# Performance work log

Measured on AMD Instinct MI355X. Metric: run time of the kernel, lower is better.

The kernel has to match this reference:

```python
import jax, jax.numpy as jnp
import numpy as np

F_DIM = 2
L_LEVELS = 16
N_MIN, N_MAX = 16, 2048
_B = np.exp((np.log(N_MAX) - np.log(N_MIN)) / (L_LEVELS - 1))
NL = np.array([int(np.floor(N_MIN * _B ** l)) for l in range(L_LEVELS)], dtype=np.float32)
T_SIZE = 2 ** 19
AABB = 3.0
N_PTS = 262144
N_FREQ_DIR = 4  # direction PE frequencies -> 3 + 3*2*4 = 27 dims (matches color_MLP input 16+27)
PIS = np.array([1, 2654435761, 805459861], dtype=np.uint32)
# 8 cube-corner offsets; order matches the torch vertex enumeration
OFFS = np.array([[0,0,0],[1,0,0],[0,1,0],[1,1,0],[0,0,1],[1,0,1],[0,1,1],[1,1,1]], dtype=np.float32)


def _hash_encode(xn, tables):
    # xn: [N,3] normalized positions in ~[0,1); tables: [L,T,F]
    Ns = jnp.asarray(NL)                                   # [L]
    scaled = xn[None, :, :] * Ns[:, None, None]            # [L,N,3]
    fl = jnp.floor(scaled)
    loc = scaled - fl                                      # [L,N,3] trilinear weights
    offs_i = jnp.asarray(OFFS, jnp.int32)                  # [8,3]
    verts = fl.astype(jnp.int32)[:, :, None, :] + offs_i[None, None]   # [L,N,8,3]
    v = verts.astype(jnp.uint32)
    pis = jnp.asarray(PIS)
    h = ((v[..., 0] * pis[0]) ^ (v[..., 1] * pis[1]) ^ (v[..., 2] * pis[2])) % jnp.uint32(T_SIZE)
    idx = h.astype(jnp.int32)                              # [L,N,8]
    corner = jax.vmap(lambda t, i: t[i])(tables, idx)      # [L,N,8,F] hashed gather
    offs = jnp.asarray(OFFS)                               # [8,3]
    w = jnp.prod(offs[None, None] * loc[:, :, None, :] + (1.0 - offs[None, None]) * (1.0 - loc[:, :, None, :]), axis=-1)  # [L,N,8]
    feats = jnp.einsum('lnc,lncf->lnf', w, corner)         # [L,N,F]
    N = xn.shape[0]
    return feats.transpose(1, 0, 2).reshape(N, L_LEVELS * F_DIM)  # [N, L*F]


def _pos_enc_dir(d):
    outs = [d]
    for j in range(N_FREQ_DIR):
        outs.append(jnp.sin((2.0 ** j) * d))
        outs.append(jnp.cos((2.0 ** j) * d))
    return jnp.concatenate(outs, axis=1)                   # [N,27]


def setup_inputs() -> dict:
    key = jax.random.key(0)
    ks = jax.random.split(key, 12)
    x = jax.random.normal(ks[0], (N_PTS, 3), jnp.float32)
    d = jax.random.normal(ks[1], (N_PTS, 3), jnp.float32)
    tables = (jax.random.uniform(ks[2], (L_LEVELS, T_SIZE, F_DIM), jnp.float32) * 2.0 - 1.0) * 1e-4
    def lin(k, fi, fo):
        return jax.random.normal(k, (fi, fo), jnp.float32) * (1.0 / np.sqrt(fi))
    return {
        'x': x, 'd': d, 'tables': tables,
        'dW1': lin(ks[3], 32, 64), 'db1': jnp.zeros((64,), jnp.float32),
        'dW2': lin(ks[4], 64, 16), 'db2': jnp.zeros((16,), jnp.float32),
        'cW1': lin(ks[5], 43, 64), 'cb1': jnp.zeros((64,), jnp.float32),
        'cW2': lin(ks[6], 64, 64), 'cb2': jnp.zeros((64,), jnp.float32),
        'cW3': lin(ks[7], 64, 3), 'cb3': jnp.zeros((3,), jnp.float32),
    }


def reference(x, d, tables, dW1, db1, dW2, db2, cW1, cb1, cW2, cb2, cW3, cb3):
    xn = x / AABB
    mask = (jnp.abs(xn[:, 0]) < 0.5) & (jnp.abs(xn[:, 1]) < 0.5) & (jnp.abs(xn[:, 2]) < 0.5)
    xn = xn + 0.5
    feats = _hash_encode(xn, tables)                        # [N,32]
    h = jnp.maximum(feats @ dW1 + db1, 0.0) @ dW2 + db2     # [N,16]
    d_enc = _pos_enc_dir(d)                                 # [N,27]
    ch = jnp.concatenate([h, d_enc], axis=1)                # [N,43]
    ch = jnp.maximum(ch @ cW1 + cb1, 0.0)
    ch = jnp.maximum(ch @ cW2 + cb2, 0.0)
    rgb = jax.nn.sigmoid(ch @ cW3 + cb3)                    # [N,3]
    sigma = jnp.where(mask, h[:, 0], jnp.float32(-100000.0))
    rgb = jnp.where(mask[:, None], rgb, 0.0)
    return rgb, jnp.exp(sigma)
```

## Files before the change

### kernel.cpp

```cpp
#include <hip/hip_runtime.h>

#define NPTS 262144
#define HP1 2654435761u
#define HP2 805459861u
#define TMASK 0x7FFFFu

typedef __attribute__((ext_vector_type(8))) short short8;
typedef __attribute__((ext_vector_type(4))) float f32x4;
typedef unsigned short ushort_t;
typedef unsigned int uint_t;

#define MFMA(a, b, c) __builtin_amdgcn_mfma_f32_16x16x32_bf16((a), (b), (c), 0, 0, 0)

__device__ __forceinline__ ushort_t f2bf(float f) {
    uint_t u = __float_as_uint(f);
    return (ushort_t)((u + 0x7FFFu + ((u >> 16) & 1u)) >> 16);
}
__device__ __forceinline__ float sigmoidf_fast(float v) {
    return 1.0f / (1.0f + __expf(-v));
}

#define DOFF0 0
#define DOFF1 4913
#define DOFF2 17080
#define DOFF3 46871
#define DOFF4 126378
#define DTOT  331757

#define WS_DN_OFF (16u * 1024u * 1024u)
#define WS_WF_OFF (22u * 1024u * 1024u)

#define OFF_DW1 0
#define OFF_DW2 2048
#define OFF_CW1 3072
#define OFF_CW2 7168
#define OFF_CW3 11264
#define WF_TOTAL 12288

extern "C" __global__ void ngp_prep(
    const float* __restrict__ dW1, const float* __restrict__ dW2,
    const float* __restrict__ cW1, const float* __restrict__ cW2,
    const float* __restrict__ cW3, ushort_t* __restrict__ wf)
{
    const int e = blockIdx.x * 256 + (int)threadIdx.x;
    if (e >= WF_TOTAL) return;
    const float* W; int base, NT, KR, NR;
    if (e < OFF_DW2)      { W = dW1; base = OFF_DW1; NT = 4; KR = 32; NR = 64; }
    else if (e < OFF_CW1) { W = dW2; base = OFF_DW2; NT = 1; KR = 64; NR = 16; }
    else if (e < OFF_CW2) { W = cW1; base = OFF_CW1; NT = 4; KR = 43; NR = 64; }
    else if (e < OFF_CW3) { W = cW2; base = OFF_CW2; NT = 4; KR = 64; NR = 64; }
    else                  { W = cW3; base = OFF_CW3; NT = 1; KR = 64; NR = 3;  }
    const int r = e - base;
    const int frag = r >> 9;
    const int lane = (r >> 3) & 63;
    const int j = r & 7;
    const int kc = frag / NT, nt = frag % NT;
    const int k = kc * 32 + ((lane >> 4) << 3) + j;
    const int n = nt * 16 + (lane & 15);
    const float v = (k < KR && n < NR) ? W[k * NR + n] : 0.0f;
    wf[e] = f2bf(v);
}

extern "C" __global__ void ngp_dense(
    const float* __restrict__ tbl, f32x4* __restrict__ dense)
{
    const int e = blockIdx.x * 256 + (int)threadIdx.x;
    if (e >= DTOT) return;
    int l, base, dim;
    if (e < DOFF1)      { l = 0; base = DOFF0; dim = 17; }
    else if (e < DOFF2) { l = 1; base = DOFF1; dim = 23; }
    else if (e < DOFF3) { l = 2; base = DOFF2; dim = 31; }
    else if (e < DOFF4) { l = 3; base = DOFF3; dim = 43; }
    else                { l = 4; base = DOFF4; dim = 59; }
    const int r = e - base;
    const int v0 = r % dim;
    const int t  = r / dim;
    const int v1 = t % dim;
    const int v2 = t / dim;
    const float2* tp = (const float2*)tbl + ((size_t)l << 19);
    const unsigned hy = (unsigned)v1 * HP1;
    const unsigned hz = (unsigned)v2 * HP2;
    const unsigned h0 = ((unsigned)v0 ^ hy ^ hz) & TMASK;
    const unsigned h1 = (((unsigned)v0 + 1u) ^ hy ^ hz) & TMASK;
    const float2 c0 = tp[h0];
    const float2 c1 = tp[h1];
    dense[e] = (f32x4){c0.x, c0.y, c1.x, c1.y};
}

extern "C" __global__ void __launch_bounds__(256) ngp_encode(
    const float* __restrict__ xin, const float* __restrict__ tbl,
    const f32x4* __restrict__ dense, uint_t* __restrict__ feats)
{
    const int b  = blockIdx.x;
    const int l  = b >> 10;
    const int pt = ((b & 1023) << 8) + (int)threadIdx.x;

    static const float NLs[16] = {16.f, 22.f, 30.f, 42.f, 58.f, 80.f, 111.f, 153.f,
                                  212.f, 294.f, 406.f, 561.f, 776.f, 1072.f, 1482.f, 2048.f};
    static const int DDIM[5] = {17, 23, 31, 43, 59};
    static const int DOFFS[5] = {DOFF0, DOFF1, DOFF2, DOFF3, DOFF4};

    const float x0 = xin[3 * pt + 0];
    const float x1 = xin[3 * pt + 1];
    const float x2 = xin[3 * pt + 2];
    const bool msk = (fabsf(x0) < 1.5f) & (fabsf(x1) < 1.5f) & (fabsf(x2) < 1.5f);
    if (!msk) return;

    const float nl = NLs[l];
    const float s0 = (x0 / 3.0f + 0.5f) * nl;
    const float s1 = (x1 / 3.0f + 0.5f) * nl;
    const float s2 = (x2 / 3.0f + 0.5f) * nl;
    const float f0 = floorf(s0), f1 = floorf(s1), f2 = floorf(s2);
    const float l0 = s0 - f0, l1 = s1 - f1, l2 = s2 - f2;
    const float m0 = 1.0f - l0, m1 = 1.0f - l1, m2 = 1.0f - l2;

    float a = 0.0f, bb = 0.0f;

    if (l < 5) {
        const int dim = DDIM[l];
        const f32x4* dp = dense + DOFFS[l];
        const int idx = ((int)f2 * dim + (int)f1) * dim + (int)f0;
        const f32x4 C00 = dp[idx];
        const f32x4 C10 = dp[idx + dim];
        const f32x4 C01 = dp[idx + dim * dim];
        const f32x4 C11 = dp[idx + dim * dim + dim];
        float w;
        w = m1 * m2; a = fmaf(m0 * w, C00[0], a); bb = fmaf(m0 * w, C00[1], bb);
                     a = fmaf(l0 * w, C00[2], a); bb = fmaf(l0 * w, C00[3], bb);
        w = l1 * m2; a = fmaf(m0 * w, C10[0], a); bb = fmaf(m0 * w, C10[1], bb);
                     a = fmaf(l0 * w, C10[2], a); bb = fmaf(l0 * w, C10[3], bb);
        w = m1 * l2; a = fmaf(m0 * w, C01[0], a); bb = fmaf(m0 * w, C01[1], bb);
                     a = fmaf(l0 * w, C01[2], a); bb = fmaf(l0 * w, C01[3], bb);
        w = l1 * l2; a = fmaf(m0 * w, C11[0], a); bb = fmaf(m0 * w, C11[1], bb);
                     a = fmaf(l0 * w, C11[2], a); bb = fmaf(l0 * w, C11[3], bb);
    } else {
        const float2* tp = (const float2*)tbl + ((size_t)l << 19);
        const f32x4* tp4 = (const f32x4*)tp;
        const unsigned v0 = (unsigned)(int)f0;
        const unsigned hy0 = (unsigned)(int)f1 * HP1, hy1 = hy0 + HP1;
        const unsigned hz0 = (unsigned)(int)f2 * HP2, hz1 = hz0 + HP2;
        unsigned hyz[4];
        hyz[0] = hy0 ^ hz0;
        hyz[1] = hy1 ^ hz0;
        hyz[2] = hy0 ^ hz1;
        hyz[3] = hy1 ^ hz1;

        float2 c[8];
        if ((v0 & 1u) == 0u) {
            #pragma unroll
            for (int j = 0; j < 4; ++j) {
                const unsigned hp = (v0 ^ hyz[j]) & TMASK;
                const f32x4 blk = tp4[hp >> 1];
                const float2 lo = {blk[0], blk[1]};
                const float2 hi = {blk[2], blk[3]};
                const bool sw = (hp & 1u) != 0u;
                c[2 * j + 0] = sw ? hi : lo;
                c[2 * j + 1] = sw ? lo : hi;
            }
        } else {
            const unsigned vb0 = v0 + 1u;
            #pragma unroll
            for (int j = 0; j < 4; ++j) {
                c[2 * j + 0] = tp[(v0  ^ hyz[j]) & TMASK];
                c[2 * j + 1] = tp[(vb0 ^ hyz[j]) & TMASK];
            }
        }
        float w;
        w = m1 * m2; a = fmaf(m0 * w, c[0].x, a); bb = fmaf(m0 * w, c[0].y, bb);
                     a = fmaf(l0 * w, c[1].x, a); bb = fmaf(l0 * w, c[1].y, bb);
        w = l1 * m2; a = fmaf(m0 * w, c[2].x, a); bb = fmaf(m0 * w, c[2].y, bb);
                     a = fmaf(l0 * w, c[3].x, a); bb = fmaf(l0 * w, c[3].y, bb);
        w = m1 * l2; a = fmaf(m0 * w, c[4].x, a); bb = fmaf(m0 * w, c[4].y, bb);
                     a = fmaf(l0 * w, c[5].x, a); bb = fmaf(l0 * w, c[5].y, bb);
        w = l1 * l2; a = fmaf(m0 * w, c[6].x, a); bb = fmaf(m0 * w, c[6].y, bb);
                     a = fmaf(l0 * w, c[7].x, a); bb = fmaf(l0 * w, c[7].y, bb);
    }

    feats[(size_t)l * NPTS + pt] = (uint_t)f2bf(a) | ((uint_t)f2bf(bb) << 16);
}

extern "C" __global__ void __launch_bounds__(256) ngp_mlp(
    const float* __restrict__ xin, const float* __restrict__ din,
    const uint_t* __restrict__ featsbf, const ushort_t* __restrict__ wf,
    const float* __restrict__ db1, const float* __restrict__ db2,
    const float* __restrict__ cb1, const float* __restrict__ cb2,
    const float* __restrict__ cb3,
    float* __restrict__ out)
{
    __shared__ short act[4][4096];
    __shared__ float mk[4][64];

    const int w    = (int)threadIdx.x >> 6;
    const int lane = (int)threadIdx.x & 63;
    const int lrow = lane & 15;
    const int lq   = lane >> 4;
    const int ptb  = blockIdx.x * 256 + w * 64;
    const int p    = ptb + lane;
    char* Ab = (char*)&act[w][0];

#define LDSA(mt, kc) (*reinterpret_cast<const short8*>(Ab + ((((mt) * 16 + lrow) * 128 + (kc) * 64 + lq * 16) ^ ((lrow & 7) << 4))))
#define LOADB(off)   (*reinterpret_cast<const short8*>(wf + (off) + lane * 8))
#define STB16(row, col, val) *reinterpret_cast<ushort_t*>(Ab + ((((row) * 128 + (col) * 2)) ^ (((row) & 7) << 4))) = (val)

    const float x0 = xin[3 * p + 0];
    const float x1 = xin[3 * p + 1];
    const float x2 = xin[3 * p + 2];
    const bool msk = (fabsf(x0) < 1.5f) & (fabsf(x1) < 1.5f) & (fabsf(x2) < 1.5f);
    mk[w][lane] = msk ? 1.0f : 0.0f;

    uint_t u[16];
    #pragma unroll
    for (int l = 0; l < 16; ++l) u[l] = featsbf[(size_t)l * NPTS + p];
    #pragma unroll
    for (int c = 0; c < 4; ++c) {
        short8 v;
        #pragma unroll
        for (int q = 0; q < 4; ++q) {
            v[2 * q + 0] = (short)(u[4 * c + q] & 0xFFFFu);
            v[2 * q + 1] = (short)(u[4 * c + q] >> 16);
        }
        const int byte = (lane * 128 + 16 * c) ^ ((lane & 7) << 4);
        *reinterpret_cast<short8*>(Ab + byte) = v;
    }
    const float d0v = din[3 * p + 0];
    const float d1v = din[3 * p + 1];
    const float d2v = din[3 * p + 2];

    __syncthreads();

    f32x4 acc[4][4];
    #pragma unroll
    for (int nt = 0; nt < 4; ++nt) {
        const float b = db1[nt * 16 + lrow];
        #pragma unroll
        for (int mt = 0; mt < 4; ++mt) acc[mt][nt] = (f32x4){b, b, b, b};
    }
    {
        short8 a0 = LDSA(0, 0), a1 = LDSA(1, 0), a2 = LDSA(2, 0), a3 = LDSA(3, 0);
        #pragma unroll
        for (int nt = 0; nt < 4; ++nt) {
            const short8 B = LOADB(OFF_DW1 + nt * 512);
            acc[0][nt] = MFMA(a0, B, acc[0][nt]);
            acc[1][nt] = MFMA(a1, B, acc[1][nt]);
            acc[2][nt] = MFMA(a2, B, acc[2][nt]);
            acc[3][nt] = MFMA(a3, B, acc[3][nt]);
        }
    }
    __syncthreads();
    #pragma unroll
    for (int mt = 0; mt < 4; ++mt)
        #pragma unroll
        for (int nt = 0; nt < 4; ++nt)
            #pragma unroll
            for (int r = 0; r < 4; ++r) {
                const int row = mt * 16 + lq * 4 + r;
                STB16(row, nt * 16 + lrow, f2bf(fmaxf(acc[mt][nt][r], 0.0f)));
            }
    __syncthreads();

    f32x4 hD[4];
    {
        const float b = db2[lrow];
        #pragma unroll
        for (int mt = 0; mt < 4; ++mt) hD[mt] = (f32x4){b, b, b, b};
        #pragma unroll
        for (int kc = 0; kc < 2; ++kc) {
            const short8 B = LOADB(OFF_DW2 + kc * 512);
            #pragma unroll
            for (int mt = 0; mt < 4; ++mt) hD[mt] = MFMA(LDSA(mt, kc), B, hD[mt]);
        }
    }
    __syncthreads();

    if (lrow == 0) {
        #pragma unroll
        for (int mt = 0; mt < 4; ++mt)
            #pragma unroll
            for (int r = 0; r < 4; ++r) {
                const int row = mt * 16 + lq * 4 + r;
                const float mm = mk[w][row];
                out[3 * NPTS + ptb + row] = (mm != 0.0f) ? __expf(hD[mt][r]) : 0.0f;
            }
    }
    #pragma unroll
    for (int mt = 0; mt < 4; ++mt)
        #pragma unroll
        for (int r = 0; r < 4; ++r) {
            const int row = mt * 16 + lq * 4 + r;
            STB16(row, lrow, f2bf(hD[mt][r]));
        }
    {
        ushort_t t[48];
        t[0] = f2bf(d0v); t[1] = f2bf(d1v); t[2] = f2bf(d2v);
        #pragma unroll
        for (int j = 0; j < 4; ++j) {
            const float s = (float)(1 << j);
            t[3 + 6 * j + 0] = f2bf(__sinf(s * d0v));
            t[3 + 6 * j + 1] = f2bf(__sinf(s * d1v));
            t[3 + 6 * j + 2] = f2bf(__sinf(s * d2v));
            t[3 + 6 * j + 3] = f2bf(__cosf(s * d0v));
            t[3 + 6 * j + 4] = f2bf(__cosf(s * d1v));
            t[3 + 6 * j + 5] = f2bf(__cosf(s * d2v));
        }
        #pragma unroll
        for (int i = 27; i < 48; ++i) t[i] = 0;
        #pragma unroll
        for (int c = 0; c < 6; ++c) {
            short8 v;
            #pragma unroll
            for (int j = 0; j < 8; ++j) v[j] = (short)t[8 * c + j];
            const int byte = (lane * 128 + 32 + 16 * c) ^ ((lane & 7) << 4);
            *reinterpret_cast<short8*>(Ab + byte) = v;
        }
    }
    __syncthreads();

    #pragma unroll
    for (int nt = 0; nt < 4; ++nt) {
        const float b = cb1[nt * 16 + lrow];
        #pragma unroll
        for (int mt = 0; mt < 4; ++mt) acc[mt][nt] = (f32x4){b, b, b, b};
    }
    #pragma unroll
    for (int kc = 0; kc < 2; ++kc) {
        short8 a0 = LDSA(0, kc), a1 = LDSA(1, kc), a2 = LDSA(2, kc), a3 = LDSA(3, kc);
        #pragma unroll
        for (int nt = 0; nt < 4; ++nt) {
            const short8 B = LOADB(OFF_CW1 + (kc * 4 + nt) * 512);
            acc[0][nt] = MFMA(a0, B, acc[0][nt]);
            acc[1][nt] = MFMA(a1, B, acc[1][nt]);
            acc[2][nt] = MFMA(a2, B, acc[2][nt]);
            acc[3][nt] = MFMA(a3, B, acc[3][nt]);
        }
    }
    __syncthreads();
    #pragma unroll
    for (int mt = 0; mt < 4; ++mt)
        #pragma unroll
        for (int nt = 0; nt < 4; ++nt)
            #pragma unroll
            for (int r = 0; r < 4; ++r) {
                const int row = mt * 16 + lq * 4 + r;
                STB16(row, nt * 16 + lrow, f2bf(fmaxf(acc[mt][nt][r], 0.0f)));
            }
    __syncthreads();

    #pragma unroll
    for (int nt = 0; nt < 4; ++nt) {
        const float b = cb2[nt * 16 + lrow];
        #pragma unroll
        for (int mt = 0; mt < 4; ++mt) acc[mt][nt] = (f32x4){b, b, b, b};
    }
    #pragma unroll
    for (int kc = 0; kc < 2; ++kc) {
        short8 a0 = LDSA(0, kc), a1 = LDSA(1, kc), a2 = LDSA(2, kc), a3 = LDSA(3, kc);
        #pragma unroll
        for (int nt = 0; nt < 4; ++nt) {
            const short8 B = LOADB(OFF_CW2 + (kc * 4 + nt) * 512);
            acc[0][nt] = MFMA(a0, B, acc[0][nt]);
            acc[1][nt] = MFMA(a1, B, acc[1][nt]);
            acc[2][nt] = MFMA(a2, B, acc[2][nt]);
            acc[3][nt] = MFMA(a3, B, acc[3][nt]);
        }
    }
    __syncthreads();
    #pragma unroll
    for (int mt = 0; mt < 4; ++mt)
        #pragma unroll
        for (int nt = 0; nt < 4; ++nt)
            #pragma unroll
            for (int r = 0; r < 4; ++r) {
                const int row = mt * 16 + lq * 4 + r;
                STB16(row, nt * 16 + lrow, f2bf(fmaxf(acc[mt][nt][r], 0.0f)));
            }
    __syncthreads();

    f32x4 rD[4];
    {
        const float b = (lrow < 3) ? cb3[lrow] : 0.0f;
        #pragma unroll
        for (int mt = 0; mt < 4; ++mt) rD[mt] = (f32x4){b, b, b, b};
        #pragma unroll
        for (int kc = 0; kc < 2; ++kc) {
            const short8 B = LOADB(OFF_CW3 + kc * 512);
            #pragma unroll
            for (int mt = 0; mt < 4; ++mt) rD[mt] = MFMA(LDSA(mt, kc), B, rD[mt]);
        }
    }
    if (lrow < 3) {
        #pragma unroll
        for (int mt = 0; mt < 4; ++mt)
            #pragma unroll
            for (int r = 0; r < 4; ++r) {
                const int row = mt * 16 + lq * 4 + r;
                const float mm = mk[w][row];
                out[3 * (ptb + row) + lrow] = (mm != 0.0f) ? sigmoidf_fast(rD[mt][r]) : 0.0f;
            }
    }
#undef LDSA
#undef LOADB
#undef STB16
}

extern "C" void kernel_launch(void* const* d_in, const int* in_sizes, int n_in,
                              void* d_out, int out_size, void* d_ws, size_t ws_size,
                              hipStream_t stream) {
    const float* x    = (const float*)d_in[0];
    const float* d    = (const float*)d_in[1];
    const float* tbl  = (const float*)d_in[2];
    const float* dW1  = (const float*)d_in[3];
    const float* db1  = (const float*)d_in[4];
    const float* dW2  = (const float*)d_in[5];
    const float* db2  = (const float*)d_in[6];
    const float* cW1  = (const float*)d_in[7];
    const float* cb1  = (const float*)d_in[8];
    const float* cW2  = (const float*)d_in[9];
    const float* cb2  = (const float*)d_in[10];
    const float* cW3  = (const float*)d_in[11];
    const float* cb3  = (const float*)d_in[12];

    uint_t* feats = (uint_t*)d_ws;
    f32x4* dense  = (f32x4*)((char*)d_ws + WS_DN_OFF);
    ushort_t* wfr = (ushort_t*)((char*)d_ws + WS_WF_OFF);

    ngp_prep<<<48, 256, 0, stream>>>(dW1, dW2, cW1, cW2, cW3, wfr);
    ngp_dense<<<(DTOT + 255) / 256, 256, 0, stream>>>(tbl, dense);
    ngp_encode<<<16 * 1024, 256, 0, stream>>>(x, tbl, dense, feats);
    ngp_mlp<<<NPTS / 256, 256, 0, stream>>>(
        x, d, feats, wfr, db1, db2, cb1, cb2, cb3, (float*)d_out);
}
```

Measured before the change: 112.5 us.

## Merge prep and dense kernels, simplify hashed gather, use one-wave MLP blocks

The weight-fragment prep kernel and the dense-grid build kernel become a single launch, with blocks split by index, which saves one kernel launch. The hashed-level gather drops the paired 16-byte load path that relied on x-parity and goes back to eight independent float2 loads, which shortens code and removes divergence. The MLP kernel now runs 64-thread blocks, one wave each, with its own LDS tile, replacing 256-thread blocks that held four waves. Using more, smaller blocks may change occupancy and scheduling, and the simpler gather gives up the adjacent-pair load saving.

```diff
diff --git a/kernel.cpp b/kernel.cpp
--- a/kernel.cpp
+++ b/kernel.cpp
@@ -26,6 +26,7 @@
 #define DOFF3 46871
 #define DOFF4 126378
 #define DTOT  331757
+#define DENSE_BLOCKS 1296
 
 #define WS_DN_OFF (16u * 1024u * 1024u)
 #define WS_WF_OFF (22u * 1024u * 1024u)
@@ -36,35 +37,35 @@
 #define OFF_CW2 7168
 #define OFF_CW3 11264
 #define WF_TOTAL 12288
-
-extern "C" __global__ void ngp_prep(
+#define PREP_BLOCKS 48
+
+extern "C" __global__ void ngp_predense(
     const float* __restrict__ dW1, const float* __restrict__ dW2,
     const float* __restrict__ cW1, const float* __restrict__ cW2,
-    const float* __restrict__ cW3, ushort_t* __restrict__ wf)
-{
-    const int e = blockIdx.x * 256 + (int)threadIdx.x;
-    if (e >= WF_TOTAL) return;
-    const float* W; int base, NT, KR, NR;
-    if (e < OFF_DW2)      { W = dW1; base = OFF_DW1; NT = 4; KR = 32; NR = 64; }
-    else if (e < OFF_CW1) { W = dW2; base = OFF_DW2; NT = 1; KR = 64; NR = 16; }
-    else if (e < OFF_CW2) { W = cW1; base = OFF_CW1; NT = 4; KR = 43; NR = 64; }
-    else if (e < OFF_CW3) { W = cW2; base = OFF_CW2; NT = 4; KR = 64; NR = 64; }
-    else                  { W = cW3; base = OFF_CW3; NT = 1; KR = 64; NR = 3;  }
-    const int r = e - base;
-    const int frag = r >> 9;
-    const int lane = (r >> 3) & 63;
-    const int j = r & 7;
-    const int kc = frag / NT, nt = frag % NT;
-    const int k = kc * 32 + ((lane >> 4) << 3) + j;
-    const int n = nt * 16 + (lane & 15);
-    const float v = (k < KR && n < NR) ? W[k * NR + n] : 0.0f;
-    wf[e] = f2bf(v);
-}
-
-extern "C" __global__ void ngp_dense(
+    const float* __restrict__ cW3, ushort_t* __restrict__ wf,
     const float* __restrict__ tbl, f32x4* __restrict__ dense)
 {
-    const int e = blockIdx.x * 256 + (int)threadIdx.x;
+    if (blockIdx.x < PREP_BLOCKS) {
+        const int e = blockIdx.x * 256 + (int)threadIdx.x;
+        if (e >= WF_TOTAL) return;
+        const float* W; int base, NT, KR, NR;
+        if (e < OFF_DW2)      { W = dW1; base = OFF_DW1; NT = 4; KR = 32; NR = 64; }
+        else if (e < OFF_CW1) { W = dW2; base = OFF_DW2; NT = 1; KR = 64; NR = 16; }
+        else if (e < OFF_CW2) { W = cW1; base = OFF_CW1; NT = 4; KR = 43; NR = 64; }
+        else if (e < OFF_CW3) { W = cW2; base = OFF_CW2; NT = 4; KR = 64; NR = 64; }
+        else                  { W = cW3; base = OFF_CW3; NT = 1; KR = 64; NR = 3;  }
+        const int r = e - base;
+        const int frag = r >> 9;
+        const int lane = (r >> 3) & 63;
+        const int j = r & 7;
+        const int kc = frag / NT, nt = frag % NT;
+        const int k = kc * 32 + ((lane >> 4) << 3) + j;
+        const int n = nt * 16 + (lane & 15);
+        const float v = (k < KR && n < NR) ? W[k * NR + n] : 0.0f;
+        wf[e] = f2bf(v);
+        return;
+    }
+    const int e = (blockIdx.x - PREP_BLOCKS) * 256 + (int)threadIdx.x;
     if (e >= DTOT) return;
     int l, base, dim;
     if (e < DOFF1)      { l = 0; base = DOFF0; dim = 17; }
@@ -135,51 +136,32 @@
                      a = fmaf(l0 * w, C11[2], a); bb = fmaf(l0 * w, C11[3], bb);
     } else {
         const float2* tp = (const float2*)tbl + ((size_t)l << 19);
-        const f32x4* tp4 = (const f32x4*)tp;
-        const unsigned v0 = (unsigned)(int)f0;
-        const unsigned hy0 = (unsigned)(int)f1 * HP1, hy1 = hy0 + HP1;
-        const unsigned hz0 = (unsigned)(int)f2 * HP2, hz1 = hz0 + HP2;
-        unsigned hyz[4];
-        hyz[0] = hy0 ^ hz0;
-        hyz[1] = hy1 ^ hz0;
-        hyz[2] = hy0 ^ hz1;
-        hyz[3] = hy1 ^ hz1;
-
-        float2 c[8];
-        if ((v0 & 1u) == 0u) {
-            #pragma unroll
-            for (int j = 0; j < 4; ++j) {
-                const unsigned hp = (v0 ^ hyz[j]) & TMASK;
-                const f32x4 blk = tp4[hp >> 1];
-                const float2 lo = {blk[0], blk[1]};
-                const float2 hi = {blk[2], blk[3]};
-                const bool sw = (hp & 1u) != 0u;
-                c[2 * j + 0] = sw ? hi : lo;
-                c[2 * j + 1] = sw ? lo : hi;
-            }
-        } else {
-            const unsigned vb0 = v0 + 1u;
-            #pragma unroll
-            for (int j = 0; j < 4; ++j) {
-                c[2 * j + 0] = tp[(v0  ^ hyz[j]) & TMASK];
-                c[2 * j + 1] = tp[(vb0 ^ hyz[j]) & TMASK];
-            }
-        }
+        const unsigned va0 = (unsigned)(int)f0, vb0 = va0 + 1u;
+        const unsigned va1 = (unsigned)(int)f1 * HP1, vb1 = va1 + HP1;
+        const unsigned va2 = (unsigned)(int)f2 * HP2, vb2 = va2 + HP2;
+        const float2 c0 = tp[(va0 ^ va1 ^ va2) & TMASK];
+        const float2 c1 = tp[(vb0 ^ va1 ^ va2) & TMASK];
+        const float2 c2 = tp[(va0 ^ vb1 ^ va2) & TMASK];
+        const float2 c3 = tp[(vb0 ^ vb1 ^ va2) & TMASK];
+        const float2 c4 = tp[(va0 ^ va1 ^ vb2) & TMASK];
+        const float2 c5 = tp[(vb0 ^ va1 ^ vb2) & TMASK];
+        const float2 c6 = tp[(va0 ^ vb1 ^ vb2) & TMASK];
+        const float2 c7 = tp[(vb0 ^ vb1 ^ vb2) & TMASK];
         float w;
-        w = m1 * m2; a = fmaf(m0 * w, c[0].x, a); bb = fmaf(m0 * w, c[0].y, bb);
-                     a = fmaf(l0 * w, c[1].x, a); bb = fmaf(l0 * w, c[1].y, bb);
-        w = l1 * m2; a = fmaf(m0 * w, c[2].x, a); bb = fmaf(m0 * w, c[2].y, bb);
-                     a = fmaf(l0 * w, c[3].x, a); bb = fmaf(l0 * w, c[3].y, bb);
-        w = m1 * l2; a = fmaf(m0 * w, c[4].x, a); bb = fmaf(m0 * w, c[4].y, bb);
-                     a = fmaf(l0 * w, c[5].x, a); bb = fmaf(l0 * w, c[5].y, bb);
-        w = l1 * l2; a = fmaf(m0 * w, c[6].x, a); bb = fmaf(m0 * w, c[6].y, bb);
-                     a = fmaf(l0 * w, c[7].x, a); bb = fmaf(l0 * w, c[7].y, bb);
+        w = m1 * m2; a = fmaf(m0 * w, c0.x, a); bb = fmaf(m0 * w, c0.y, bb);
+                     a = fmaf(l0 * w, c1.x, a); bb = fmaf(l0 * w, c1.y, bb);
+        w = l1 * m2; a = fmaf(m0 * w, c2.x, a); bb = fmaf(m0 * w, c2.y, bb);
+                     a = fmaf(l0 * w, c3.x, a); bb = fmaf(l0 * w, c3.y, bb);
+        w = m1 * l2; a = fmaf(m0 * w, c4.x, a); bb = fmaf(m0 * w, c4.y, bb);
+                     a = fmaf(l0 * w, c5.x, a); bb = fmaf(l0 * w, c5.y, bb);
+        w = l1 * l2; a = fmaf(m0 * w, c6.x, a); bb = fmaf(m0 * w, c6.y, bb);
+                     a = fmaf(l0 * w, c7.x, a); bb = fmaf(l0 * w, c7.y, bb);
     }
 
     feats[(size_t)l * NPTS + pt] = (uint_t)f2bf(a) | ((uint_t)f2bf(bb) << 16);
 }
 
-extern "C" __global__ void __launch_bounds__(256) ngp_mlp(
+extern "C" __global__ void __launch_bounds__(64) ngp_mlp(
     const float* __restrict__ xin, const float* __restrict__ din,
     const uint_t* __restrict__ featsbf, const ushort_t* __restrict__ wf,
     const float* __restrict__ db1, const float* __restrict__ db2,
@@ -187,16 +169,15 @@
     const float* __restrict__ cb3,
     float* __restrict__ out)
 {
-    __shared__ short act[4][4096];
-    __shared__ float mk[4][64];
-
-    const int w    = (int)threadIdx.x >> 6;
-    const int lane = (int)threadIdx.x & 63;
+    __shared__ short act[4096];
+    __shared__ float mk[64];
+
+    const int lane = (int)threadIdx.x;
     const int lrow = lane & 15;
     const int lq   = lane >> 4;
-    const int ptb  = blockIdx.x * 256 + w * 64;
+    const int ptb  = blockIdx.x * 64;
     const int p    = ptb + lane;
-    char* Ab = (char*)&act[w][0];
+    char* Ab = (char*)&act[0];
 
 #define LDSA(mt, kc) (*reinterpret_cast<const short8*>(Ab + ((((mt) * 16 + lrow) * 128 + (kc) * 64 + lq * 16) ^ ((lrow & 7) << 4))))
 #define LOADB(off)   (*reinterpret_cast<const short8*>(wf + (off) + lane * 8))
@@ -206,7 +187,7 @@
     const float x1 = xin[3 * p + 1];
     const float x2 = xin[3 * p + 2];
     const bool msk = (fabsf(x0) < 1.5f) & (fabsf(x1) < 1.5f) & (fabsf(x2) < 1.5f);
-    mk[w][lane] = msk ? 1.0f : 0.0f;
+    mk[lane] = msk ? 1.0f : 0.0f;
 
     uint_t u[16];
     #pragma unroll
@@ -278,8 +259,7 @@
             #pragma unroll
             for (int r = 0; r < 4; ++r) {
                 const int row = mt * 16 + lq * 4 + r;
-                const float mm = mk[w][row];
-                out[3 * NPTS + ptb + row] = (mm != 0.0f) ? __expf(hD[mt][r]) : 0.0f;
+                out[3 * NPTS + ptb + row] = (mk[row] != 0.0f) ? __expf(hD[mt][r]) : 0.0f;
             }
     }
     #pragma unroll
@@ -393,8 +373,7 @@
             #pragma unroll
             for (int r = 0; r < 4; ++r) {
                 const int row = mt * 16 + lq * 4 + r;
-                const float mm = mk[w][row];
-                out[3 * (ptb + row) + lrow] = (mm != 0.0f) ? sigmoidf_fast(rD[mt][r]) : 0.0f;
+                out[3 * (ptb + row) + lrow] = (mk[row] != 0.0f) ? sigmoidf_fast(rD[mt][r]) : 0.0f;
             }
     }
 #undef LDSA
@@ -423,9 +402,9 @@
     f32x4* dense  = (f32x4*)((char*)d_ws + WS_DN_OFF);
     ushort_t* wfr = (ushort_t*)((char*)d_ws + WS_WF_OFF);
 
-    ngp_prep<<<48, 256, 0, stream>>>(dW1, dW2, cW1, cW2, cW3, wfr);
-    ngp_dense<<<(DTOT + 255) / 256, 256, 0, stream>>>(tbl, dense);
+    ngp_predense<<<PREP_BLOCKS + DENSE_BLOCKS, 256, 0, stream>>>(
+        dW1, dW2, cW1, cW2, cW3, wfr, tbl, dense);
     ngp_encode<<<16 * 1024, 256, 0, stream>>>(x, tbl, dense, feats);
-    ngp_mlp<<<NPTS / 256, 256, 0, stream>>>(
+    ngp_mlp<<<NPTS / 64, 64, 0, stream>>>(
         x, d, feats, wfr, db1, db2, cb1, cb2, cb3, (float*)d_out);
 }
```

Result: faster. 108.3 us (-3.8%).
